# Kernel tuning notes

Hardware: AMD Instinct MI355X
Metric: run time of the kernel (lower is better)

## Reference

```python
import jax, jax.numpy as jnp
import numpy as np

K = 3            # kernel_size
PAD = (K - 1) // 2
UM = 2           # um_dim
C_IN = 128
C_OUT = 128
SLOPE = 0.01     # F.leaky_relu default negative slope


def setup_inputs() -> dict:
    key = jax.random.key(0)
    k1, k2, k3 = jax.random.split(key, 3)
    xx = jax.random.normal(k1, (16, C_IN, 64, 64), dtype=jnp.float32)
    # Conv2d(C_in, C_out, K, stride=K, bias=True) parameters
    w = jax.random.normal(k2, (C_OUT, C_IN, K, K), dtype=jnp.float32) * 0.05
    b = jax.random.normal(k3, (C_OUT,), dtype=jnp.float32) * 0.05
    return {"xx": xx, "w": w, "b": b}


def reference(xx, w, b):
    B, C, H, Wd = xx.shape
    # --- unfold: replicate pad, then extract all KxK patches (stride 1) ---
    xp = jnp.pad(xx, ((0, 0), (0, 0), (PAD, PAD), (PAD, PAD)), mode="edge")
    # patches[b, c, r, s, i, j] = xp[b, c, i + r, j + s]   -> [B, C, K, K, H, W]
    patches = jnp.stack(
        [jnp.stack([xp[:, :, r:r + H, s:s + Wd] for s in range(K)], axis=2)
         for r in range(K)], axis=2)
    # --- subtract per-(um-slot, pixel) mean over channel groups and KxK ---
    g = patches.reshape(B, C // UM, UM, K, K, H, Wd)
    avgs = g.mean(axis=(1, 3, 4), keepdims=True)        # [B,1,UM,1,1,H,W]
    g = g - avgs
    p = g.reshape(B, C, K, K, H, Wd)
    # --- patch-wise conv (kernel_size == stride on the tiled image). The
    # torch code's transpose(2,4).transpose(-1,-2) tiling places patch col
    # offset s along tiled rows and row offset r along tiled cols, so the
    # conv weight w[o,c,r,s] pairs with patches[b,c,s,r,i,j]. ---
    out = jnp.einsum("ocrs,bcsrij->boij", w, p) + b[None, :, None, None]
    # leaky_relu
    out = jnp.where(out > 0, out, SLOPE * out)
    # --- add mean back per um-slot ---
    m = avgs[:, :, :, 0, 0]                             # [B,1,UM,H,W]
    O = out.shape[1]
    out = out.reshape(B, O // UM, UM, H, Wd) + m
    return out.reshape(B, O, H, Wd)
```

## Files before the change

kernel.cpp:

```cpp
#include <hip/hip_runtime.h>
#include <hip/hip_bf16.h>

typedef __bf16 bf16x8 __attribute__((ext_vector_type(8)));
typedef float  f32x4  __attribute__((ext_vector_type(4)));

#define NB 16
#define CI 128
#define CO 128
#define HH 64
#define WW 64

#define SCOLS 66
#define SPIX  (6 * SCOLS)
#define QSZ   ((size_t)NB * HH * WW * 32)

#define GLDS16(gp, lp) __builtin_amdgcn_global_load_lds( \
    (const __attribute__((address_space(1))) unsigned int*)(const void*)(gp), \
    (__attribute__((address_space(3))) unsigned int*)(void*)(lp), 16, 0, 0)

__global__ void prep(const float* __restrict__ x, const float* __restrict__ w,
                     __bf16* __restrict__ Ag, float* __restrict__ wsum,
                     __bf16* __restrict__ xT, float* __restrict__ S) {
    __shared__ float tile[128 * 65];
    __shared__ float red[8];
    const int blk = blockIdx.x, tid = threadIdx.x;
    if (blk < 1024) {
        const int bb = blk >> 6, y = blk & 63;
        const float* xr = x + ((size_t)bb * CI) * (HH * WW) + y * WW;
        for (int idx = tid; idx < 2048; idx += 256) {
            int c = idx >> 4, x4 = idx & 15;
            float4 v = *(const float4*)(xr + (size_t)c * (HH * WW) + x4 * 4);
            *(float4*)(tile + c * 65 + x4 * 4) = v;
        }
        __syncthreads();
        for (int idx = tid; idx < 1024; idx += 256) {
            int px = idx >> 4, cg = idx & 15;
            bf16x8 o8;
            #pragma unroll
            for (int j = 0; j < 8; ++j)
                o8[j] = (__bf16)tile[(cg * 8 + j) * 65 + px];
            __bf16* dst = xT + (size_t)(cg >> 2) * QSZ
                        + (((size_t)bb * 64 + y) * 64 + px) * 32 + (cg & 3) * 8;
            *(bf16x8*)dst = o8;
        }
        if (tid < 64) {
            float se = 0.f, so = 0.f;
            #pragma unroll 8
            for (int c = 0; c < 128; c += 2) {
                se += tile[c * 65 + tid];
                so += tile[(c + 1) * 65 + tid];
            }
            float2 v = {se, so};
            *(float2*)(S + (((size_t)bb * 64 + y) * 64 + tid) * 2) = v;
        }
    } else if (blk < 1096) {
        int gid  = (blk - 1024) * 256 + tid;
        int l    = gid & 63;
        int frag = gid >> 6;
        int mt   = frag & 7;
        int t    = frag >> 3;
        int tap  = t >> 2;
        int r    = tap % 3;
        int s    = tap / 3;
        int o    = mt * 16 + (l & 15);
        int cb   = (t & 3) * 32 + (l >> 4) * 8;
        bf16x8 v;
        #pragma unroll
        for (int j = 0; j < 8; ++j)
            v[j] = (__bf16)w[((o * CI + cb + j) * 3 + r) * 3 + s];
        *(bf16x8*)(Ag + (size_t)gid * 8) = v;
    } else {
        int o = blk - 1096;
        const float* p = w + (size_t)o * CI * 9;
        float se = 0.f, so = 0.f;
        for (int idx = tid; idx < CI * 9; idx += 256) {
            int c = idx / 9;
            float v = p[idx];
            if (c & 1) so += v; else se += v;
        }
        #pragma unroll
        for (int off = 32; off; off >>= 1) {
            se += __shfl_down(se, off);
            so += __shfl_down(so, off);
        }
        int wv = tid >> 6, lane = tid & 63;
        if (lane == 0) { red[wv * 2] = se; red[wv * 2 + 1] = so; }
        __syncthreads();
        if (tid == 0) {
            wsum[o]      = red[0] + red[2] + red[4] + red[6];
            wsum[CO + o] = red[1] + red[3] + red[5] + red[7];
        }
    }
}

__global__ __launch_bounds__(512, 2) void conv_main(
        const __bf16* __restrict__ xT,
        const float* __restrict__ S,
        const float* __restrict__ bias,
        const float* __restrict__ wsum,
        const __bf16* __restrict__ Ag,
        float* __restrict__ out)
{
    __shared__ __align__(16) __bf16 Alds[9 * 4096];
    __shared__ __align__(16) __bf16 slab[2][SPIX * 32];
    __shared__ float SrowS[6 * 64 * 2];
    __shared__ float avgl[512];

    const int tid  = threadIdx.x;
    const int b    = blockIdx.y;
    const int row0 = blockIdx.x * 4;

    const int wave = tid >> 6, lane = tid & 63;
    const int wm = wave >> 2;
    const int wn = wave & 3;
    const int m = lane & 15, qv = lane >> 4;

    auto issue_A = [&](int qn, int a0, int a1) {
        for (int a = a0 + wave; a < a1; a += 8) {
            int tap = a >> 3, part = a & 7;
            const __bf16* gp = Ag
                + (((size_t)((tap * 4 + qn) * 8 + part)) << 9) + (lane << 3);
            GLDS16(gp, &Alds[(size_t)a << 9]);
        }
    };
    auto issue_slab = [&](int qn, __bf16* dst) {
        for (int c = wave; c < 25; c += 8) {
            int p   = c * 16 + (lane >> 2);
            int r   = (p * 993) >> 16;
            int col = p - r * 66;
            int yi  = row0 - 1 + r; yi = yi < 0 ? 0 : (yi > 63 ? 63 : yi);
            int xi  = col - 1;      xi = xi < 0 ? 0 : (xi > 63 ? 63 : xi);
            const __bf16* gp = xT + (size_t)qn * QSZ
                + (((size_t)b * 64 + yi) * 64 + xi) * 32 + (lane & 3) * 8;
            if (p < SPIX) GLDS16(gp, dst + ((size_t)c << 9));
        }
    };

    issue_slab(0, slab[0]);
    issue_A(0, 0, 72);
    for (int idx = tid; idx < 768; idx += 512) {
        int r = idx >> 7, rem = idx & 127;
        int col = rem >> 1, uu = idx & 1;
        int yi = row0 - 1 + r; yi = yi < 0 ? 0 : (yi > 63 ? 63 : yi);
        SrowS[idx] = S[(((size_t)b * 64 + yi) * 64 + col) * 2 + uu];
    }
    __syncthreads();
    {
        int rr = tid >> 7, col = (tid >> 1) & 63, uu = tid & 1;
        float ssum = 0.f;
        #pragma unroll
        for (int dy = 0; dy < 3; ++dy)
            #pragma unroll
            for (int dx = 0; dx < 3; ++dx) {
                int cc = col - 1 + dx; cc = cc < 0 ? 0 : (cc > 63 ? 63 : cc);
                ssum += SrowS[((rr + dy) * 64 + cc) * 2 + uu];
            }
        avgl[tid] = ssum * (1.0f / 576.0f);
    }

    f32x4 acc[4][4];
    #pragma unroll
    for (int i = 0; i < 4; ++i)
        #pragma unroll
        for (int j = 0; j < 4; ++j)
            acc[i][j] = (f32x4){0.f, 0.f, 0.f, 0.f};

    int bbase[4];
    #pragma unroll
    for (int nt = 0; nt < 4; ++nt)
        bbase[nt] = (wn * SCOLS + nt * 16 + m) * 32 + qv * 8;
    const __bf16* Aw = Alds + (wm * 4) * 512 + lane * 8;

    for (int q = 0; q < 4; ++q) {
        const __bf16* sl = slab[q & 1];
        if (q < 3) issue_slab(q + 1, slab[(q + 1) & 1]);
        #pragma unroll
        for (int tap = 0; tap < 4; ++tap) {
            const int s_ = tap / 3, r3 = tap % 3;
            const int poff = (s_ * SCOLS + r3) * 32;
            bf16x8 Bf[4], Af[4];
            #pragma unroll
            for (int nt = 0; nt < 4; ++nt)
                Bf[nt] = *(const bf16x8*)(sl + bbase[nt] + poff);
            #pragma unroll
            for (int i = 0; i < 4; ++i)
                Af[i] = *(const bf16x8*)(Aw + (tap * 8 + i) * 512);
            #pragma unroll
            for (int i = 0; i < 4; ++i)
                #pragma unroll
                for (int nt = 0; nt < 4; ++nt)
                    acc[i][nt] = __builtin_amdgcn_mfma_f32_16x16x32_bf16(
                        Af[i], Bf[nt], acc[i][nt], 0, 0, 0);
        }
        __syncthreads();
        if (q < 3) issue_A(q + 1, 0, 32);
        #pragma unroll
        for (int tap = 4; tap < 9; ++tap) {
            const int s_ = tap / 3, r3 = tap % 3;
            const int poff = (s_ * SCOLS + r3) * 32;
            bf16x8 Bf[4], Af[4];
            #pragma unroll
            for (int nt = 0; nt < 4; ++nt)
                Bf[nt] = *(const bf16x8*)(sl + bbase[nt] + poff);
            #pragma unroll
            for (int i = 0; i < 4; ++i)
                Af[i] = *(const bf16x8*)(Aw + (tap * 8 + i) * 512);
            #pragma unroll
            for (int i = 0; i < 4; ++i)
                #pragma unroll
                for (int nt = 0; nt < 4; ++nt)
                    acc[i][nt] = __builtin_amdgcn_mfma_f32_16x16x32_bf16(
                        Af[i], Bf[nt], acc[i][nt], 0, 0, 0);
        }
        __syncthreads();
        if (q < 3) issue_A(q + 1, 32, 72);
    }

    float a0v[4], a1v[4];
    #pragma unroll
    for (int nt = 0; nt < 4; ++nt) {
        int col = nt * 16 + m;
        a0v[nt] = avgl[wn * 128 + col * 2 + 0];
        a1v[nt] = avgl[wn * 128 + col * 2 + 1];
    }
    float* outb = out + (size_t)b * CO * HH * WW + (size_t)(row0 + wn) * WW;
    #pragma unroll
    for (int i = 0; i < 4; ++i) {
        #pragma unroll
        for (int rg = 0; rg < 4; ++rg) {
            int o = wm * 64 + i * 16 + qv * 4 + rg;
            float bo = bias[o];
            float w0 = wsum[o];
            float w1 = wsum[CO + o];
            float* po = outb + (size_t)o * (HH * WW);
            #pragma unroll
            for (int nt = 0; nt < 4; ++nt) {
                float v = acc[i][nt][rg] + bo - a0v[nt] * w0 - a1v[nt] * w1;
                v = v > 0.f ? v : 0.01f * v;
                v += (o & 1) ? a1v[nt] : a0v[nt];
                __builtin_nontemporal_store(v, po + nt * 16 + m);
            }
        }
    }
}

extern "C" void kernel_launch(void* const* d_in, const int* in_sizes, int n_in,
                              void* d_out, int out_size, void* d_ws, size_t ws_size,
                              hipStream_t stream) {
    const float* x    = (const float*)d_in[0];
    const float* w    = (const float*)d_in[1];
    const float* bias = (const float*)d_in[2];
    float* out = (float*)d_out;

    __bf16* Ag   = (__bf16*)d_ws;
    float*  wsum = (float*)((char*)d_ws + 294912);
    __bf16* xT   = (__bf16*)((char*)d_ws + 295936);
    float*  S    = (float*)((char*)d_ws + 295936 + 2 * QSZ * 4);

    prep<<<1224, 256, 0, stream>>>(x, w, Ag, wsum, xT, S);

    dim3 grid(HH / 4, NB);
    conv_main<<<grid, 512, 0, stream>>>(xT, S, bias, wsum, Ag, out);
}
```

Baseline: 113.1 us.

## Load B fragments directly from global into registers, stage weights via registers

Removes the LDS slab of input pixels and the async global-to-LDS copies. Each wave now reads its B fragments straight from global memory (relying on L1/L2 for the halo reuse) with a 3-step register prefetch pipeline. Weights are loaded into registers and written to LDS between chunks, guarded by two barriers. The prep transpose loop is also reshaped to a fixed per-thread mapping. This trades LDS traffic and occupancy pressure for more global/cache loads, higher register use, and serialized barriers around weight refills.

```diff
diff --git a/kernel.cpp b/kernel.cpp
--- a/kernel.cpp
+++ b/kernel.cpp
@@ -9,14 +9,7 @@
 #define CO 128
 #define HH 64
 #define WW 64
-
-#define SCOLS 66
-#define SPIX  (6 * SCOLS)
-#define QSZ   ((size_t)NB * HH * WW * 32)
-
-#define GLDS16(gp, lp) __builtin_amdgcn_global_load_lds( \
-    (const __attribute__((address_space(1))) unsigned int*)(const void*)(gp), \
-    (__attribute__((address_space(3))) unsigned int*)(void*)(lp), 16, 0, 0)
+#define QSZ ((size_t)NB * HH * WW * 32)
 
 __global__ void prep(const float* __restrict__ x, const float* __restrict__ w,
                      __bf16* __restrict__ Ag, float* __restrict__ wsum,
@@ -33,15 +26,15 @@
             *(float4*)(tile + c * 65 + x4 * 4) = v;
         }
         __syncthreads();
-        for (int idx = tid; idx < 1024; idx += 256) {
-            int px = idx >> 4, cg = idx & 15;
+        const int cg4 = tid & 3, px = (tid >> 2) & 63;
+        #pragma unroll
+        for (int k = 0; k < 4; ++k) {
             bf16x8 o8;
             #pragma unroll
             for (int j = 0; j < 8; ++j)
-                o8[j] = (__bf16)tile[(cg * 8 + j) * 65 + px];
-            __bf16* dst = xT + (size_t)(cg >> 2) * QSZ
-                        + (((size_t)bb * 64 + y) * 64 + px) * 32 + (cg & 3) * 8;
-            *(bf16x8*)dst = o8;
+                o8[j] = (__bf16)tile[((k * 4 + cg4) * 8 + j) * 65 + px];
+            *(bf16x8*)(xT + (size_t)k * QSZ
+                       + (((size_t)bb * 64 + y) * 64 + px) * 32 + cg4 * 8) = o8;
         }
         if (tid < 64) {
             float se = 0.f, so = 0.f;
@@ -102,7 +95,6 @@
         float* __restrict__ out)
 {
     __shared__ __align__(16) __bf16 Alds[9 * 4096];
-    __shared__ __align__(16) __bf16 slab[2][SPIX * 32];
     __shared__ float SrowS[6 * 64 * 2];
     __shared__ float avgl[512];
 
@@ -115,29 +107,12 @@
     const int wn = wave & 3;
     const int m = lane & 15, qv = lane >> 4;
 
-    auto issue_A = [&](int qn, int a0, int a1) {
-        for (int a = a0 + wave; a < a1; a += 8) {
-            int tap = a >> 3, part = a & 7;
-            const __bf16* gp = Ag
-                + (((size_t)((tap * 4 + qn) * 8 + part)) << 9) + (lane << 3);
-            GLDS16(gp, &Alds[(size_t)a << 9]);
-        }
-    };
-    auto issue_slab = [&](int qn, __bf16* dst) {
-        for (int c = wave; c < 25; c += 8) {
-            int p   = c * 16 + (lane >> 2);
-            int r   = (p * 993) >> 16;
-            int col = p - r * 66;
-            int yi  = row0 - 1 + r; yi = yi < 0 ? 0 : (yi > 63 ? 63 : yi);
-            int xi  = col - 1;      xi = xi < 0 ? 0 : (xi > 63 ? 63 : xi);
-            const __bf16* gp = xT + (size_t)qn * QSZ
-                + (((size_t)b * 64 + yi) * 64 + xi) * 32 + (lane & 3) * 8;
-            if (p < SPIX) GLDS16(gp, dst + ((size_t)c << 9));
-        }
-    };
-
-    issue_slab(0, slab[0]);
-    issue_A(0, 0, 72);
+    bf16x8 Areg[9];
+    #pragma unroll
+    for (int k = 0; k < 9; ++k)
+        Areg[k] = *(const bf16x8*)(Ag + (((size_t)((k * 4 + 0) * 8 + wave)) << 9)
+                                      + (lane << 3));
+
     for (int idx = tid; idx < 768; idx += 512) {
         int r = idx >> 7, rem = idx & 127;
         int col = rem >> 1, uu = idx & 1;
@@ -157,6 +132,25 @@
             }
         avgl[tid] = ssum * (1.0f / 576.0f);
     }
+    #pragma unroll
+    for (int k = 0; k < 9; ++k)
+        *(bf16x8*)(Alds + (((size_t)(k * 8 + wave)) << 9) + (lane << 3)) = Areg[k];
+
+    int boffs[4][3];
+    #pragma unroll
+    for (int nt = 0; nt < 4; ++nt)
+        #pragma unroll
+        for (int r3 = 0; r3 < 3; ++r3) {
+            int xi = nt * 16 + m - 1 + r3;
+            xi = xi < 0 ? 0 : (xi > 63 ? 63 : xi);
+            boffs[nt][r3] = xi * 32 + qv * 8;
+        }
+    size_t rowbase[3];
+    #pragma unroll
+    for (int s_ = 0; s_ < 3; ++s_) {
+        int yi = row0 + wn - 1 + s_; yi = yi < 0 ? 0 : (yi > 63 ? 63 : yi);
+        rowbase[s_] = ((size_t)b * 64 + yi) << 11;
+    }
 
     f32x4 acc[4][4];
     #pragma unroll
@@ -165,55 +159,55 @@
         for (int j = 0; j < 4; ++j)
             acc[i][j] = (f32x4){0.f, 0.f, 0.f, 0.f};
 
-    int bbase[4];
-    #pragma unroll
-    for (int nt = 0; nt < 4; ++nt)
-        bbase[nt] = (wn * SCOLS + nt * 16 + m) * 32 + qv * 8;
-    const __bf16* Aw = Alds + (wm * 4) * 512 + lane * 8;
-
+    bf16x8 Bv[4][4];
+    #pragma unroll
+    for (int st = 0; st < 3; ++st) {
+        const int s_ = st / 3, r3 = st % 3;
+        #pragma unroll
+        for (int nt = 0; nt < 4; ++nt)
+            Bv[st & 3][nt] = *(const bf16x8*)(xT + rowbase[s_] + boffs[nt][r3]);
+    }
+    __syncthreads();
+
+    #pragma unroll
     for (int q = 0; q < 4; ++q) {
-        const __bf16* sl = slab[q & 1];
-        if (q < 3) issue_slab(q + 1, slab[(q + 1) & 1]);
-        #pragma unroll
-        for (int tap = 0; tap < 4; ++tap) {
-            const int s_ = tap / 3, r3 = tap % 3;
-            const int poff = (s_ * SCOLS + r3) * 32;
-            bf16x8 Bf[4], Af[4];
-            #pragma unroll
-            for (int nt = 0; nt < 4; ++nt)
-                Bf[nt] = *(const bf16x8*)(sl + bbase[nt] + poff);
+        if (q < 3) {
+            #pragma unroll
+            for (int k = 0; k < 9; ++k)
+                Areg[k] = *(const bf16x8*)(Ag
+                    + (((size_t)((k * 4 + q + 1) * 8 + wave)) << 9) + (lane << 3));
+        }
+        #pragma unroll
+        for (int tap = 0; tap < 9; ++tap) {
+            const int st = q * 9 + tap;
+            if (st + 3 < 36) {
+                const int s2 = st + 3, q2 = s2 / 9, t2 = s2 % 9;
+                const int ss = t2 / 3, rr3 = t2 % 3;
+                #pragma unroll
+                for (int nt = 0; nt < 4; ++nt)
+                    Bv[s2 & 3][nt] = *(const bf16x8*)(xT + (size_t)q2 * QSZ
+                        + rowbase[ss] + boffs[nt][rr3]);
+            }
+            bf16x8 Af[4];
             #pragma unroll
             for (int i = 0; i < 4; ++i)
-                Af[i] = *(const bf16x8*)(Aw + (tap * 8 + i) * 512);
+                Af[i] = *(const bf16x8*)(Alds
+                    + (((size_t)(tap * 8 + wm * 4 + i)) << 9) + (lane << 3));
             #pragma unroll
             for (int i = 0; i < 4; ++i)
                 #pragma unroll
                 for (int nt = 0; nt < 4; ++nt)
                     acc[i][nt] = __builtin_amdgcn_mfma_f32_16x16x32_bf16(
-                        Af[i], Bf[nt], acc[i][nt], 0, 0, 0);
-        }
-        __syncthreads();
-        if (q < 3) issue_A(q + 1, 0, 32);
-        #pragma unroll
-        for (int tap = 4; tap < 9; ++tap) {
-            const int s_ = tap / 3, r3 = tap % 3;
-            const int poff = (s_ * SCOLS + r3) * 32;
-            bf16x8 Bf[4], Af[4];
-            #pragma unroll
-            for (int nt = 0; nt < 4; ++nt)
-                Bf[nt] = *(const bf16x8*)(sl + bbase[nt] + poff);
-            #pragma unroll
-            for (int i = 0; i < 4; ++i)
-                Af[i] = *(const bf16x8*)(Aw + (tap * 8 + i) * 512);
-            #pragma unroll
-            for (int i = 0; i < 4; ++i)
-                #pragma unroll
-                for (int nt = 0; nt < 4; ++nt)
-                    acc[i][nt] = __builtin_amdgcn_mfma_f32_16x16x32_bf16(
-                        Af[i], Bf[nt], acc[i][nt], 0, 0, 0);
-        }
-        __syncthreads();
-        if (q < 3) issue_A(q + 1, 32, 72);
+                        Af[i], Bv[st & 3][nt], acc[i][nt], 0, 0, 0);
+        }
+        if (q < 3) {
+            __syncthreads();
+            #pragma unroll
+            for (int k = 0; k < 9; ++k)
+                *(bf16x8*)(Alds + (((size_t)(k * 8 + wave)) << 9)
+                           + (lane << 3)) = Areg[k];
+            __syncthreads();
+        }
     }
 
     float a0v[4], a1v[4];
```

Measured after the change: 117.9 us. 4.2% more time.
